# Kernel tuning notes

Measured on AMD Instinct MI355X. Metric: run time of the kernel, lower is better.

The kernel has to match this reference:

```python
import jax, jax.numpy as jnp
import numpy as np

D_MODEL = 1024
N_HEADS = 16
HEAD_D = D_MODEL // N_HEADS  # 64
B, T = 4, 4096
ROPE_BASE = 10000.0


def _rope(x):
    # Standard interleaved RoPE over the full feature dim (module applies RoPE
    # to q,k after reshaping back to (B,T,D)).
    Bx, Tx, Dx = x.shape
    half = Dx // 2
    inv_freq = 1.0 / (ROPE_BASE ** (jnp.arange(half, dtype=jnp.float32) / half))
    ang = jnp.arange(Tx, dtype=jnp.float32)[:, None] * inv_freq[None, :]  # (T, half)
    cos, sin = jnp.cos(ang), jnp.sin(ang)
    x1 = x[..., 0::2]
    x2 = x[..., 1::2]
    r1 = x1 * cos - x2 * sin
    r2 = x1 * sin + x2 * cos
    # interleave back
    out = jnp.stack([r1, r2], axis=-1).reshape(Bx, Tx, Dx)
    return out


def setup_inputs() -> dict:
    key = jax.random.key(0)
    k_x, k_q, k_k, k_v = jax.random.split(key, 4)
    x = jax.random.normal(k_x, (B, T, D_MODEL), dtype=jnp.float32)
    # kaiming_uniform on (d, d, n_heads): fan_in = d*n_heads, bound = sqrt(6/fan_in)
    bound = np.sqrt(6.0 / (HEAD_D * N_HEADS))
    shp = (HEAD_D, HEAD_D, N_HEADS)
    w_q = jax.random.uniform(k_q, shp, jnp.float32, -bound, bound)
    w_k = jax.random.uniform(k_k, shp, jnp.float32, -bound, bound)
    w_v = jax.random.uniform(k_v, shp, jnp.float32, -bound, bound)
    return {"x": x, "w_q": w_q, "w_k": w_k, "w_v": w_v}


def reference(x, w_q, w_k, w_v):
    Bx, Tx, Dx = x.shape
    d = Dx // N_HEADS
    xh = x.reshape(Bx, Tx, d, N_HEADS)  # (B,T,d,h)
    q = jnp.einsum('btqh,qdh->btdh', xh, w_q).reshape(Bx, Tx, Dx)
    k = jnp.einsum('btkh,kdh->btdh', xh, w_k).reshape(Bx, Tx, Dx)
    v = jnp.einsum('btvh,vdh->btdh', xh, w_v).reshape(Bx, Tx, Dx)
    q = _rope(q)
    k = _rope(k)
    gamma = 1.0 / jnp.sqrt(jnp.float32(Dx))
    scores = jnp.einsum('bqd,bkd->bqk', q, k) * gamma  # contracts FULL D (single map)
    causal = jnp.tril(jnp.ones((Tx, Tx), dtype=bool))
    scores = jnp.where(causal[None], scores, -jnp.inf)
    attn = jax.nn.softmax(scores, axis=-1)
    y = jnp.einsum('bqt,btd->bqd', attn, v)
    return y
```

## Files before the change

kernel.cpp:

```cpp
#include <hip/hip_runtime.h>
#include <cmath>

#define B_ 4
#define T_ 4096
#define D_ 1024

typedef __attribute__((ext_vector_type(4))) float f32x4;
typedef __attribute__((ext_vector_type(2))) float f32x2;
typedef __attribute__((ext_vector_type(8))) short s16x8;

__device__ __forceinline__ f32x4 mfma_bf16(s16x8 a, s16x8 b, f32x4 c) {
    return __builtin_amdgcn_mfma_f32_16x16x32_bf16(a, b, c, 0, 0, 0);
}
__device__ __forceinline__ unsigned short f2bf(float f) {
    union { float f; unsigned int u; } v; v.f = f;
    unsigned int r = v.u + 0x7FFFu + ((v.u >> 16) & 1u);
    return (unsigned short)(r >> 16);
}
template <int CTRL>
__device__ __forceinline__ float dppf(float x) {
    return __int_as_float(
        __builtin_amdgcn_mov_dpp(__float_as_int(x), CTRL, 0xF, 0xF, true));
}
__device__ __forceinline__ float rowmax16(float v) {
    v = fmaxf(v, dppf<0xB1>(v));
    v = fmaxf(v, dppf<0x4E>(v));
    v = fmaxf(v, dppf<0x141>(v));
    v = fmaxf(v, dppf<0x140>(v));
    return v;
}
__device__ __forceinline__ float rowsum16(float v) {
    v += dppf<0xB1>(v);
    v += dppf<0x4E>(v);
    v += dppf<0x141>(v);
    v += dppf<0x140>(v);
    return v;
}

__global__ __launch_bounds__(256) void k_wtrans(const float* __restrict__ wq,
                                                const float* __restrict__ wk,
                                                const float* __restrict__ wv,
                                                unsigned short* __restrict__ wt) {
    int p = blockIdx.x >> 4;
    int h = blockIdx.x & 15;
    const float* src = (p == 0) ? wq : (p == 1) ? wk : wv;
    unsigned short* dst = wt + (size_t)((p * 16 + h) * 64) * 64;
    for (int idx = threadIdx.x; idx < 64 * 64; idx += 256) {
        int d = idx >> 6, i = idx & 63;
        dst[d * 64 + i] = f2bf(src[i * 1024 + d * 16 + h]);
    }
}

__global__ __launch_bounds__(256, 3) void k_qkv(const float* __restrict__ x,
                                             const unsigned short* __restrict__ wt,
                                             unsigned short* __restrict__ Qt,
                                             unsigned short* __restrict__ Kt,
                                             unsigned short* __restrict__ Vt) {
    int bid = blockIdx.x;
    int hp  = bid >> 8;
    int b   = (bid >> 6) & 3;
    int tc  = bid & 63;
    int t0  = tc * 64;
    int tid = threadIdx.x, w = tid >> 6, lane = tid & 63;
    int quad = lane >> 4, l16 = lane & 15;

    __shared__ alignas(16) unsigned short xh[2 * 64 * 72];
    __shared__ alignas(16) unsigned short outl[64 * 68];

    for (int n = tid; n < 4096; n += 256) {
        int t = n >> 6, i = n & 63;
        f32x2 v = *(const f32x2*)&x[(size_t)(b * T_ + t0 + t) * D_ + i * 16 + 2 * hp];
        xh[t * 72 + i]        = f2bf(v.x);
        xh[4608 + t * 72 + i] = f2bf(v.y);
    }
    __syncthreads();

    s16x8 xf[2][2];
    #pragma unroll
    for (int hh = 0; hh < 2; ++hh)
        #pragma unroll
        for (int kc = 0; kc < 2; ++kc)
            xf[hh][kc] = *(const s16x8*)&xh[hh * 4608 + (16 * w + l16) * 72 + kc * 32 + quad * 8];

    f32x4 acc[3][2][4];
    #pragma unroll
    for (int p = 0; p < 3; ++p)
        #pragma unroll
        for (int hh = 0; hh < 2; ++hh)
            #pragma unroll
            for (int nt = 0; nt < 4; ++nt)
                acc[p][hh][nt] = (f32x4){0.f, 0.f, 0.f, 0.f};

    #pragma unroll
    for (int p = 0; p < 3; ++p)
        #pragma unroll
        for (int hh = 0; hh < 2; ++hh)
            #pragma unroll
            for (int nt = 0; nt < 4; ++nt)
                #pragma unroll
                for (int kc = 0; kc < 2; ++kc) {
                    const s16x8 wf = *(const s16x8*)&wt[
                        (size_t)((p * 16 + 2 * hp + hh) * 64 + nt * 16 + l16) * 64 + kc * 32 + quad * 8];
                    if (p < 2)
                        acc[p][hh][nt] = mfma_bf16(xf[hh][kc], wf, acc[p][hh][nt]);
                    else
                        acc[p][hh][nt] = mfma_bf16(wf, xf[hh][kc], acc[p][hh][nt]);
                }

    #pragma unroll
    for (int nt = 0; nt < 4; ++nt) {
        int d = nt * 16 + l16;
        float f = exp2f((float)(d * 8 + hp) * -0.02595256324130751f);
        #pragma unroll
        for (int r = 0; r < 4; ++r) {
            float ang = (float)(t0 + 16 * w + quad * 4 + r) * f;
            float s, c;
            __sincosf(ang, &s, &c);
            float a0 = acc[0][0][nt][r], a1 = acc[0][1][nt][r];
            acc[0][0][nt][r] = a0 * c - a1 * s;
            acc[0][1][nt][r] = a0 * s + a1 * c;
            float k0 = acc[1][0][nt][r], k1 = acc[1][1][nt][r];
            acc[1][0][nt][r] = k0 * c - k1 * s;
            acc[1][1][nt][r] = k0 * s + k1 * c;
        }
    }

    #pragma unroll
    for (int p = 0; p < 3; ++p)
        #pragma unroll
        for (int hh = 0; hh < 2; ++hh) {
            __syncthreads();
            if (p < 2) {
                #pragma unroll
                for (int nt = 0; nt < 4; ++nt)
                    #pragma unroll
                    for (int r = 0; r < 4; ++r)
                        outl[(16 * w + quad * 4 + r) * 68 + nt * 16 + l16] = f2bf(acc[p][hh][nt][r]);
            } else {
                #pragma unroll
                for (int mt = 0; mt < 4; ++mt)
                    #pragma unroll
                    for (int r = 0; r < 4; ++r)
                        outl[(mt * 16 + quad * 4 + r) * 68 + 16 * w + l16] = f2bf(acc[p][hh][mt][r]);
            }
            __syncthreads();
            int h = 2 * hp + hh;
            if (p < 2) {
                unsigned short* g = (p == 0 ? Qt : Kt) + ((size_t)(b * 16 + h) * T_ + t0) * 64;
                for (int n = 2 * tid; n < 4096; n += 512) {
                    int t = n >> 6, dd = n & 63;
                    *(unsigned int*)(g + n) = *(const unsigned int*)&outl[t * 68 + dd];
                }
            } else {
                unsigned short* g = Vt + (size_t)(b * 16 + h) * 64 * T_;
                for (int n = 2 * tid; n < 4096; n += 512) {
                    int d = n >> 6, tt = n & 63;
                    int tile = 2 * tc + (tt >> 5);
                    *(unsigned int*)(g + (size_t)tile * 2048 + d * 32 + (tt & 31)) =
                        *(const unsigned int*)&outl[d * 68 + tt];
                }
            }
        }
}

__global__ __launch_bounds__(512, 2) void k_attn(const unsigned short* __restrict__ Qt,
                                              const unsigned short* __restrict__ Kt,
                                              const unsigned short* __restrict__ Vt,
                                              float* __restrict__ out) {
    int bid = blockIdx.x;
    int b = (bid >> 1) & 3;
    int q = ((bid >> 3) & 31) * 2 + (bid & 1);
    int qt = (bid < 256) ? (127 - q) : q;
    int q0 = qt * 32;
    int tid = threadIdx.x, w = tid >> 6, lane = tid & 63;
    int quad = lane >> 4, l16 = lane & 15;

    __shared__ alignas(16) float S_red[8][32][68];
    __shared__ alignas(16) unsigned short P_lds[32][72];
    __shared__ float alpha_s[32], l_st[32];

    s16x8 qf[2][4];
    #pragma unroll
    for (int qs = 0; qs < 2; ++qs)
        #pragma unroll
        for (int c = 0; c < 4; ++c) {
            int dg = w * 128 + c * 32 + quad * 8;
            int head = dg >> 6, d64 = dg & 63;
            qf[qs][c] = *(const s16x8*)&Qt[((size_t)(b * 16 + head) * T_ + q0 + qs * 16 + l16) * 64 + d64];
        }

    f32x4 Y[8][2];
    #pragma unroll
    for (int mt = 0; mt < 8; ++mt) { Y[mt][0] = (f32x4){0,0,0,0}; Y[mt][1] = (f32x4){0,0,0,0}; }

    const float gamma = 0.03125f;
    int rq = tid >> 4;
    int kk4 = (tid & 15) * 4;
    int nkt = (qt >> 1) + 1;
    float m_reg = -INFINITY, l_reg = 0.f;

    {
        f32x4 S[4][2];
        #pragma unroll
        for (int kps = 0; kps < 4; ++kps) { S[kps][0] = (f32x4){0,0,0,0}; S[kps][1] = (f32x4){0,0,0,0}; }
        #pragma unroll
        for (int kps = 0; kps < 4; ++kps)
            #pragma unroll
            for (int c = 0; c < 4; ++c) {
                int dg = w * 128 + c * 32 + quad * 8;
                int head = dg >> 6, d64 = dg & 63;
                s16x8 kf = *(const s16x8*)&Kt[((size_t)(b * 16 + head) * T_ + kps * 16 + l16) * 64 + d64];
                S[kps][0] = mfma_bf16(kf, qf[0][c], S[kps][0]);
                S[kps][1] = mfma_bf16(kf, qf[1][c], S[kps][1]);
            }
        #pragma unroll
        for (int kps = 0; kps < 4; ++kps)
            #pragma unroll
            for (int qs = 0; qs < 2; ++qs)
                *(f32x4*)&S_red[w][qs * 16 + l16][kps * 16 + quad * 4] = S[kps][qs];
    }
    __syncthreads();

    s16x8 vfA[8];
    s16x8 vfB[8];

    for (int kt = 0; kt < nkt; ++kt) {
        int kbase = kt * 64;
        bool more = (kt + 1 < nkt);

        #pragma unroll
        for (int mt = 0; mt < 8; ++mt) {
            int dg = w * 128 + mt * 16 + l16;
            int head = dg >> 6, d64 = dg & 63;
            vfA[mt] = *(const s16x8*)&Vt[
                (((size_t)(b * 16 + head) * 128 + 2 * kt) * 64 + d64) * 32 + quad * 8];
        }

        f32x4 s = {0.f, 0.f, 0.f, 0.f};
        #pragma unroll
        for (int sl = 0; sl < 8; ++sl) {
            f32x4 v = *(const f32x4*)&S_red[sl][rq][kk4];
            s.x += v.x; s.y += v.y; s.z += v.z; s.w += v.w;
        }
        int qg = q0 + rq;
        int kb = kbase + kk4;
        s.x = (kb     > qg) ? -INFINITY : s.x * gamma;
        s.y = (kb + 1 > qg) ? -INFINITY : s.y * gamma;
        s.z = (kb + 2 > qg) ? -INFINITY : s.z * gamma;
        s.w = (kb + 3 > qg) ? -INFINITY : s.w * gamma;
        float mx = rowmax16(fmaxf(fmaxf(s.x, s.y), fmaxf(s.z, s.w)));
        float m_new = (mx > m_reg + 8.f) ? mx : m_reg;
        float alpha = __expf(m_reg - m_new);
        float p0 = __expf(s.x - m_new), p1 = __expf(s.y - m_new);
        float p2 = __expf(s.z - m_new), p3 = __expf(s.w - m_new);
        float ps = rowsum16((p0 + p1) + (p2 + p3));
        l_reg = alpha * l_reg + ps;
        m_reg = m_new;
        if ((tid & 15) == 0) alpha_s[rq] = alpha;
        unsigned int plo = (unsigned int)f2bf(p0) | ((unsigned int)f2bf(p1) << 16);
        unsigned int phi = (unsigned int)f2bf(p2) | ((unsigned int)f2bf(p3) << 16);
        *(unsigned long long*)&P_lds[rq][kk4] =
            (unsigned long long)plo | ((unsigned long long)phi << 32);
        __syncthreads();

        #pragma unroll
        for (int mt = 0; mt < 8; ++mt) {
            int dg = w * 128 + mt * 16 + l16;
            int head = dg >> 6, d64 = dg & 63;
            vfB[mt] = *(const s16x8*)&Vt[
                (((size_t)(b * 16 + head) * 128 + 2 * kt + 1) * 64 + d64) * 32 + quad * 8];
        }
        float a0 = alpha_s[l16], a1 = alpha_s[16 + l16];
        s16x8 pf0a = *(const s16x8*)&P_lds[l16][quad * 8];
        s16x8 pf0b = *(const s16x8*)&P_lds[l16][32 + quad * 8];
        s16x8 pf1a = *(const s16x8*)&P_lds[16 + l16][quad * 8];
        s16x8 pf1b = *(const s16x8*)&P_lds[16 + l16][32 + quad * 8];
        int scale = __any((a0 < 1.f) || (a1 < 1.f));
        __builtin_amdgcn_s_setprio(1);
        if (scale) {
            #pragma unroll
            for (int mt = 0; mt < 8; ++mt) { Y[mt][0] *= a0; Y[mt][1] *= a1; }
        }
        #pragma unroll
        for (int mt = 0; mt < 8; ++mt) {
            Y[mt][0] = mfma_bf16(vfA[mt], pf0a, Y[mt][0]);
            Y[mt][1] = mfma_bf16(vfA[mt], pf1a, Y[mt][1]);
        }
        #pragma unroll
        for (int mt = 0; mt < 8; ++mt) {
            Y[mt][0] = mfma_bf16(vfB[mt], pf0b, Y[mt][0]);
            Y[mt][1] = mfma_bf16(vfB[mt], pf1b, Y[mt][1]);
        }
        if (more) {
            f32x4 S[4][2];
            #pragma unroll
            for (int kps = 0; kps < 4; ++kps) { S[kps][0] = (f32x4){0,0,0,0}; S[kps][1] = (f32x4){0,0,0,0}; }
            #pragma unroll
            for (int kps = 0; kps < 4; ++kps)
                #pragma unroll
                for (int c = 0; c < 4; ++c) {
                    int dg = w * 128 + c * 32 + quad * 8;
                    int head = dg >> 6, d64 = dg & 63;
                    s16x8 kf = *(const s16x8*)&Kt[
                        ((size_t)(b * 16 + head) * T_ + kbase + 64 + kps * 16 + l16) * 64 + d64];
                    S[kps][0] = mfma_bf16(kf, qf[0][c], S[kps][0]);
                    S[kps][1] = mfma_bf16(kf, qf[1][c], S[kps][1]);
                }
            #pragma unroll
            for (int kps = 0; kps < 4; ++kps)
                #pragma unroll
                for (int qs = 0; qs < 2; ++qs)
                    *(f32x4*)&S_red[w][qs * 16 + l16][kps * 16 + quad * 4] = S[kps][qs];
        }
        __builtin_amdgcn_s_setprio(0);
        __syncthreads();
    }

    if ((tid & 15) == 0) l_st[rq] = l_reg;
    __syncthreads();
    float inv0 = 1.f / l_st[l16], inv1 = 1.f / l_st[16 + l16];
    #pragma unroll
    for (int mt = 0; mt < 8; ++mt)
        #pragma unroll
        for (int r = 0; r < 4; ++r) {
            int dg = w * 128 + mt * 16 + quad * 4 + r;
            int head = dg >> 6, d64 = dg & 63;
            int e = d64 * 16 + head;
            out[(size_t)(b * T_ + q0 + l16) * D_ + e]      = Y[mt][0][r] * inv0;
            out[(size_t)(b * T_ + q0 + 16 + l16) * D_ + e] = Y[mt][1][r] * inv1;
        }
}

extern "C" void kernel_launch(void* const* d_in, const int* in_sizes, int n_in,
                              void* d_out, int out_size, void* d_ws, size_t ws_size,
                              hipStream_t stream) {
    const float* x  = (const float*)d_in[0];
    const float* wq = (const float*)d_in[1];
    const float* wk = (const float*)d_in[2];
    const float* wv = (const float*)d_in[3];
    unsigned short* ws = (unsigned short*)d_ws;

    const size_t WT_ELEMS  = 3 * 16 * 64 * 64;
    const size_t QKV_ELEMS = (size_t)B_ * 16 * T_ * 64;
    const size_t NEED_BYTES = (WT_ELEMS + 3 * QKV_ELEMS) * sizeof(unsigned short);
    if (ws_size < NEED_BYTES) return;

    unsigned short* wt = ws;
    unsigned short* Qt = ws + WT_ELEMS;
    unsigned short* Kt = Qt + QKV_ELEMS;
    unsigned short* Vt = Kt + QKV_ELEMS;
    float* outp = (float*)d_out;

    k_wtrans<<<48, 256, 0, stream>>>(wq, wk, wv, wt);
    k_qkv<<<2048, 256, 0, stream>>>(x, wt, Qt, Kt, Vt);
    k_attn<<<512, 512, 0, stream>>>(Qt, Kt, Vt, outp);
}
```

Baseline: 704.1 us.

## Widen key tile to 128, store partial scores and P/V in fp16

The attention kernel now processes 128 keys per iteration instead of 64, halving the number of barrier-separated steps. Cross-wave partial score reduction moves from fp32 to fp16 shared memory with packed half-vector adds. The gamma scale is folded into Q during projection, and V and P switch from bf16 to fp16 so the PV product uses fp16 MFMA. The next tile's score MFMAs are interleaved with V loads. Summing partial scores in fp16 risks precision loss, and larger register use may lower occupancy.

```diff
diff --git a/kernel.cpp b/kernel.cpp
--- a/kernel.cpp
+++ b/kernel.cpp
@@ -8,14 +8,23 @@
 typedef __attribute__((ext_vector_type(4))) float f32x4;
 typedef __attribute__((ext_vector_type(2))) float f32x2;
 typedef __attribute__((ext_vector_type(8))) short s16x8;
+typedef _Float16 h16x8 __attribute__((ext_vector_type(8)));
+typedef _Float16 h16x4 __attribute__((ext_vector_type(4)));
 
 __device__ __forceinline__ f32x4 mfma_bf16(s16x8 a, s16x8 b, f32x4 c) {
     return __builtin_amdgcn_mfma_f32_16x16x32_bf16(a, b, c, 0, 0, 0);
+}
+__device__ __forceinline__ f32x4 mfma_f16(h16x8 a, h16x8 b, f32x4 c) {
+    return __builtin_amdgcn_mfma_f32_16x16x32_f16(a, b, c, 0, 0, 0);
 }
 __device__ __forceinline__ unsigned short f2bf(float f) {
     union { float f; unsigned int u; } v; v.f = f;
     unsigned int r = v.u + 0x7FFFu + ((v.u >> 16) & 1u);
     return (unsigned short)(r >> 16);
+}
+__device__ __forceinline__ unsigned short f2h(float f) {
+    union { _Float16 h; unsigned short u; } v; v.h = (_Float16)f;
+    return v.u;
 }
 template <int CTRL>
 __device__ __forceinline__ float dppf(float x) {
@@ -107,6 +116,7 @@
                         acc[p][hh][nt] = mfma_bf16(wf, xf[hh][kc], acc[p][hh][nt]);
                 }
 
+    const float GAM = 0.03125f;
     #pragma unroll
     for (int nt = 0; nt < 4; ++nt) {
         int d = nt * 16 + l16;
@@ -117,8 +127,8 @@
             float s, c;
             __sincosf(ang, &s, &c);
             float a0 = acc[0][0][nt][r], a1 = acc[0][1][nt][r];
-            acc[0][0][nt][r] = a0 * c - a1 * s;
-            acc[0][1][nt][r] = a0 * s + a1 * c;
+            acc[0][0][nt][r] = (a0 * c - a1 * s) * GAM;
+            acc[0][1][nt][r] = (a0 * s + a1 * c) * GAM;
             float k0 = acc[1][0][nt][r], k1 = acc[1][1][nt][r];
             acc[1][0][nt][r] = k0 * c - k1 * s;
             acc[1][1][nt][r] = k0 * s + k1 * c;
@@ -141,7 +151,7 @@
                 for (int mt = 0; mt < 4; ++mt)
                     #pragma unroll
                     for (int r = 0; r < 4; ++r)
-                        outl[(mt * 16 + quad * 4 + r) * 68 + 16 * w + l16] = f2bf(acc[p][hh][mt][r]);
+                        outl[(mt * 16 + quad * 4 + r) * 68 + 16 * w + l16] = f2h(acc[p][hh][mt][r]);
             }
             __syncthreads();
             int h = 2 * hp + hh;
@@ -175,9 +185,11 @@
     int tid = threadIdx.x, w = tid >> 6, lane = tid & 63;
     int quad = lane >> 4, l16 = lane & 15;
 
-    __shared__ alignas(16) float S_red[8][32][68];
-    __shared__ alignas(16) unsigned short P_lds[32][72];
+    __shared__ alignas(16) _Float16 S_red[8][32][136];
+    __shared__ alignas(16) _Float16 P_lds[32][136];
     __shared__ float alpha_s[32], l_st[32];
+
+    const _Float16* Vh = (const _Float16*)Vt;
 
     s16x8 qf[2][4];
     #pragma unroll
@@ -193,88 +205,74 @@
     #pragma unroll
     for (int mt = 0; mt < 8; ++mt) { Y[mt][0] = (f32x4){0,0,0,0}; Y[mt][1] = (f32x4){0,0,0,0}; }
 
-    const float gamma = 0.03125f;
     int rq = tid >> 4;
-    int kk4 = (tid & 15) * 4;
-    int nkt = (qt >> 1) + 1;
+    int k16 = tid & 15;
+    int kk8 = k16 * 8;
+    int nkt = (qt >> 2) + 1;
     float m_reg = -INFINITY, l_reg = 0.f;
 
-    {
-        f32x4 S[4][2];
-        #pragma unroll
-        for (int kps = 0; kps < 4; ++kps) { S[kps][0] = (f32x4){0,0,0,0}; S[kps][1] = (f32x4){0,0,0,0}; }
-        #pragma unroll
-        for (int kps = 0; kps < 4; ++kps)
-            #pragma unroll
-            for (int c = 0; c < 4; ++c) {
-                int dg = w * 128 + c * 32 + quad * 8;
-                int head = dg >> 6, d64 = dg & 63;
-                s16x8 kf = *(const s16x8*)&Kt[((size_t)(b * 16 + head) * T_ + kps * 16 + l16) * 64 + d64];
-                S[kps][0] = mfma_bf16(kf, qf[0][c], S[kps][0]);
-                S[kps][1] = mfma_bf16(kf, qf[1][c], S[kps][1]);
-            }
-        #pragma unroll
-        for (int kps = 0; kps < 4; ++kps)
-            #pragma unroll
-            for (int qs = 0; qs < 2; ++qs)
-                *(f32x4*)&S_red[w][qs * 16 + l16][kps * 16 + quad * 4] = S[kps][qs];
+    #pragma unroll
+    for (int kps = 0; kps < 8; ++kps) {
+        f32x4 S0 = (f32x4){0,0,0,0}, S1 = (f32x4){0,0,0,0};
+        #pragma unroll
+        for (int c = 0; c < 4; ++c) {
+            int dg = w * 128 + c * 32 + quad * 8;
+            int head = dg >> 6, d64 = dg & 63;
+            s16x8 kf = *(const s16x8*)&Kt[((size_t)(b * 16 + head) * T_ + kps * 16 + l16) * 64 + d64];
+            S0 = mfma_bf16(kf, qf[0][c], S0);
+            S1 = mfma_bf16(kf, qf[1][c], S1);
+        }
+        h16x4 v0 = {(_Float16)S0[0], (_Float16)S0[1], (_Float16)S0[2], (_Float16)S0[3]};
+        h16x4 v1 = {(_Float16)S1[0], (_Float16)S1[1], (_Float16)S1[2], (_Float16)S1[3]};
+        *(h16x4*)&S_red[w][l16][kps * 16 + quad * 4]      = v0;
+        *(h16x4*)&S_red[w][16 + l16][kps * 16 + quad * 4] = v1;
     }
     __syncthreads();
 
-    s16x8 vfA[8];
-    s16x8 vfB[8];
+    h16x8 vfb[2][8];
 
     for (int kt = 0; kt < nkt; ++kt) {
-        int kbase = kt * 64;
+        int kbase = kt * 128;
         bool more = (kt + 1 < nkt);
 
         #pragma unroll
         for (int mt = 0; mt < 8; ++mt) {
             int dg = w * 128 + mt * 16 + l16;
             int head = dg >> 6, d64 = dg & 63;
-            vfA[mt] = *(const s16x8*)&Vt[
-                (((size_t)(b * 16 + head) * 128 + 2 * kt) * 64 + d64) * 32 + quad * 8];
-        }
-
-        f32x4 s = {0.f, 0.f, 0.f, 0.f};
-        #pragma unroll
-        for (int sl = 0; sl < 8; ++sl) {
-            f32x4 v = *(const f32x4*)&S_red[sl][rq][kk4];
-            s.x += v.x; s.y += v.y; s.z += v.z; s.w += v.w;
-        }
+            vfb[0][mt] = *(const h16x8*)&Vh[
+                (((size_t)(b * 16 + head) * 128 + 4 * kt) * 64 + d64) * 32 + quad * 8];
+        }
+
+        h16x8 acc = *(const h16x8*)&S_red[0][rq][kk8];
+        #pragma unroll
+        for (int sl = 1; sl < 8; ++sl)
+            acc = acc + *(const h16x8*)&S_red[sl][rq][kk8];
+
+        float s[8], p[8];
         int qg = q0 + rq;
-        int kb = kbase + kk4;
-        s.x = (kb     > qg) ? -INFINITY : s.x * gamma;
-        s.y = (kb + 1 > qg) ? -INFINITY : s.y * gamma;
-        s.z = (kb + 2 > qg) ? -INFINITY : s.z * gamma;
-        s.w = (kb + 3 > qg) ? -INFINITY : s.w * gamma;
-        float mx = rowmax16(fmaxf(fmaxf(s.x, s.y), fmaxf(s.z, s.w)));
+        #pragma unroll
+        for (int i = 0; i < 8; ++i) {
+            float si = (float)acc[i];
+            s[i] = (kbase + kk8 + i > qg) ? -INFINITY : si;
+        }
+        float mx = fmaxf(fmaxf(fmaxf(s[0], s[1]), fmaxf(s[2], s[3])),
+                         fmaxf(fmaxf(s[4], s[5]), fmaxf(s[6], s[7])));
+        mx = rowmax16(mx);
         float m_new = (mx > m_reg + 8.f) ? mx : m_reg;
         float alpha = __expf(m_reg - m_new);
-        float p0 = __expf(s.x - m_new), p1 = __expf(s.y - m_new);
-        float p2 = __expf(s.z - m_new), p3 = __expf(s.w - m_new);
-        float ps = rowsum16((p0 + p1) + (p2 + p3));
+        float ps = 0.f;
+        #pragma unroll
+        for (int i = 0; i < 8; ++i) { p[i] = __expf(s[i] - m_new); ps += p[i]; }
+        ps = rowsum16(ps);
         l_reg = alpha * l_reg + ps;
         m_reg = m_new;
-        if ((tid & 15) == 0) alpha_s[rq] = alpha;
-        unsigned int plo = (unsigned int)f2bf(p0) | ((unsigned int)f2bf(p1) << 16);
-        unsigned int phi = (unsigned int)f2bf(p2) | ((unsigned int)f2bf(p3) << 16);
-        *(unsigned long long*)&P_lds[rq][kk4] =
-            (unsigned long long)plo | ((unsigned long long)phi << 32);
+        if (k16 == 0) alpha_s[rq] = alpha;
+        h16x8 pv = {(_Float16)p[0], (_Float16)p[1], (_Float16)p[2], (_Float16)p[3],
+                    (_Float16)p[4], (_Float16)p[5], (_Float16)p[6], (_Float16)p[7]};
+        *(h16x8*)&P_lds[rq][kk8] = pv;
         __syncthreads();
 
-        #pragma unroll
-        for (int mt = 0; mt < 8; ++mt) {
-            int dg = w * 128 + mt * 16 + l16;
-            int head = dg >> 6, d64 = dg & 63;
-            vfB[mt] = *(const s16x8*)&Vt[
-                (((size_t)(b * 16 + head) * 128 + 2 * kt + 1) * 64 + d64) * 32 + quad * 8];
-        }
         float a0 = alpha_s[l16], a1 = alpha_s[16 + l16];
-        s16x8 pf0a = *(const s16x8*)&P_lds[l16][quad * 8];
-        s16x8 pf0b = *(const s16x8*)&P_lds[l16][32 + quad * 8];
-        s16x8 pf1a = *(const s16x8*)&P_lds[16 + l16][quad * 8];
-        s16x8 pf1b = *(const s16x8*)&P_lds[16 + l16][32 + quad * 8];
         int scale = __any((a0 < 1.f) || (a1 < 1.f));
         __builtin_amdgcn_s_setprio(1);
         if (scale) {
@@ -282,41 +280,49 @@
             for (int mt = 0; mt < 8; ++mt) { Y[mt][0] *= a0; Y[mt][1] *= a1; }
         }
         #pragma unroll
-        for (int mt = 0; mt < 8; ++mt) {
-            Y[mt][0] = mfma_bf16(vfA[mt], pf0a, Y[mt][0]);
-            Y[mt][1] = mfma_bf16(vfA[mt], pf1a, Y[mt][1]);
-        }
-        #pragma unroll
-        for (int mt = 0; mt < 8; ++mt) {
-            Y[mt][0] = mfma_bf16(vfB[mt], pf0b, Y[mt][0]);
-            Y[mt][1] = mfma_bf16(vfB[mt], pf1b, Y[mt][1]);
-        }
-        if (more) {
-            f32x4 S[4][2];
+        for (int ksub = 0; ksub < 4; ++ksub) {
+            if (ksub < 3) {
+                #pragma unroll
+                for (int mt = 0; mt < 8; ++mt) {
+                    int dg = w * 128 + mt * 16 + l16;
+                    int head = dg >> 6, d64 = dg & 63;
+                    vfb[(ksub + 1) & 1][mt] = *(const h16x8*)&Vh[
+                        (((size_t)(b * 16 + head) * 128 + 4 * kt + ksub + 1) * 64 + d64) * 32 + quad * 8];
+                }
+            }
+            h16x8 pf0 = *(const h16x8*)&P_lds[l16][ksub * 32 + quad * 8];
+            h16x8 pf1 = *(const h16x8*)&P_lds[16 + l16][ksub * 32 + quad * 8];
+            if (more) {
+                #pragma unroll
+                for (int kk = 0; kk < 2; ++kk) {
+                    int kps = 2 * ksub + kk;
+                    f32x4 S0 = (f32x4){0,0,0,0}, S1 = (f32x4){0,0,0,0};
+                    #pragma unroll
+                    for (int c = 0; c < 4; ++c) {
+                        int dg = w * 128 + c * 32 + quad * 8;
+                        int head = dg >> 6, d64 = dg & 63;
+                        s16x8 kf = *(const s16x8*)&Kt[
+                            ((size_t)(b * 16 + head) * T_ + kbase + 128 + kps * 16 + l16) * 64 + d64];
+                        S0 = mfma_bf16(kf, qf[0][c], S0);
+                        S1 = mfma_bf16(kf, qf[1][c], S1);
+                    }
+                    h16x4 v0 = {(_Float16)S0[0], (_Float16)S0[1], (_Float16)S0[2], (_Float16)S0[3]};
+                    h16x4 v1 = {(_Float16)S1[0], (_Float16)S1[1], (_Float16)S1[2], (_Float16)S1[3]};
+                    *(h16x4*)&S_red[w][l16][kps * 16 + quad * 4]      = v0;
+                    *(h16x4*)&S_red[w][16 + l16][kps * 16 + quad * 4] = v1;
+                }
+            }
             #pragma unroll
-            for (int kps = 0; kps < 4; ++kps) { S[kps][0] = (f32x4){0,0,0,0}; S[kps][1] = (f32x4){0,0,0,0}; }
-            #pragma unroll
-            for (int kps = 0; kps < 4; ++kps)
-                #pragma unroll
-                for (int c = 0; c < 4; ++c) {
-                    int dg = w * 128 + c * 32 + quad * 8;
-                    int head = dg >> 6, d64 = dg & 63;
-                    s16x8 kf = *(const s16x8*)&Kt[
-                        ((size_t)(b * 16 + head) * T_ + kbase + 64 + kps * 16 + l16) * 64 + d64];
-                    S[kps][0] = mfma_bf16(kf, qf[0][c], S[kps][0]);
-                    S[kps][1] = mfma_bf16(kf, qf[1][c], S[kps][1]);
-                }
-            #pragma unroll
-            for (int kps = 0; kps < 4; ++kps)
-                #pragma unroll
-                for (int qs = 0; qs < 2; ++qs)
-                    *(f32x4*)&S_red[w][qs * 16 + l16][kps * 16 + quad * 4] = S[kps][qs];
+            for (int mt = 0; mt < 8; ++mt) {
+                Y[mt][0] = mfma_f16(vfb[ksub & 1][mt], pf0, Y[mt][0]);
+                Y[mt][1] = mfma_f16(vfb[ksub & 1][mt], pf1, Y[mt][1]);
+            }
         }
         __builtin_amdgcn_s_setprio(0);
         __syncthreads();
     }
 
-    if ((tid & 15) == 0) l_st[rq] = l_reg;
+    if (k16 == 0) l_st[rq] = l_reg;
     __syncthreads();
     float inv0 = 1.f / l_st[l16], inv1 = 1.f / l_st[16 + l16];
     #pragma unroll
```

Measured after the change: 714.4 us. No clear change (+1.5%).
